# Kernel optimization log

Hardware: AMD Instinct MI355X
Metric: run time of the kernel (lower is better)

The kernel has to match this reference:

```python
import jax, jax.numpy as jnp
import numpy as np
import math

# hyperparams matching init_kwargs
GAMMA_S = 0.8
GAMMA_U = 0.8
RHO_I = 0.1
RHO_T = 0.1
EPS = 1e-10
TAU_MIN = 0.005
TAU_MAX = 1.0
TAU_INIT = 0.07
GRAD_CLIP = 5.0
ETA_INIT = 0.01
ETA_MIN = 0.0001
N_STATE = 2900000
BSZ = 4096
DIM = 1024


def setup_inputs() -> dict:
    key = jax.random.key(0)
    k1, k2 = jax.random.split(key)
    imf = jax.random.normal(k1, (BSZ, DIM), jnp.float32)
    imf = imf / jnp.linalg.norm(imf, axis=1, keepdims=True)
    txf = jax.random.normal(k2, (BSZ, DIM), jnp.float32)
    txf = txf / jnp.linalg.norm(txf, axis=1, keepdims=True)
    return {
        "image_features": imf,
        "text_features": txf,
        "s_I": jnp.zeros((N_STATE,), jnp.float32),
        "s_T": jnp.zeros((N_STATE,), jnp.float32),
        "tau_I": jnp.full((N_STATE,), TAU_INIT, jnp.float32),
        "tau_T": jnp.full((N_STATE,), TAU_INIT, jnp.float32),
        "u_I": jnp.zeros((N_STATE,), jnp.float32),
        "u_T": jnp.zeros((N_STATE,), jnp.float32),
        "b_I": jnp.zeros((N_STATE,), jnp.float32),
        "b_T": jnp.zeros((N_STATE,), jnp.float32),
        "image_ids": jnp.arange(BSZ, dtype=jnp.int32),
        "text_ids": jnp.arange(BSZ, dtype=jnp.int32),
        "epoch": 5,
        "max_epoch": 30,
    }


def reference(image_features, text_features, s_I, s_T, tau_I, tau_T,
              u_I, u_T, b_I, b_T, image_ids, text_ids, epoch, max_epoch):
    B = image_features.shape[0]
    sim = jnp.einsum('id,jd->ij', image_features, text_features)  # [B,B]
    diag_sim = jnp.diagonal(sim)                                  # [B]

    tau_image = tau_I[image_ids]  # [B]
    tau_text = tau_T[text_ids]    # [B]

    image_diffs = sim - diag_sim[:, None]
    text_diffs = sim - diag_sim[None, :]
    # .detach() in torch -> stop_gradient
    idt = jax.lax.stop_gradient(image_diffs / tau_image[:, None])
    tdt = jax.lax.stop_gradient(text_diffs / tau_text[None, :])

    # max-trick state b_I / b_T: running row/col max per sample id
    old_b_I = b_I[image_ids]
    new_b_I = jnp.maximum(jnp.max(idt, axis=1), old_b_I)  # [B]
    old_b_T = b_T[text_ids]
    new_b_T = jnp.maximum(jnp.max(tdt, axis=0), old_b_T)  # [B]

    exp_image_diffs = jnp.exp(idt - new_b_I[:, None])
    exp_text_diffs = jnp.exp(tdt - new_b_T[None, :])
    g_I = jnp.sum(exp_image_diffs, axis=1, keepdims=True) / (B - 1)  # [B,1]
    g_T = jnp.sum(exp_text_diffs, axis=0, keepdims=True) / (B - 1)   # [1,B]

    # moving-average s state (compute_last=False, last_g_* = None path)
    s_I_new = (1.0 - GAMMA_S) * s_I[image_ids] * jnp.exp(old_b_I - new_b_I) + GAMMA_S * g_I[:, 0]
    s_T_new = (1.0 - GAMMA_S) * s_T[text_ids] * jnp.exp(old_b_T - new_b_T) + GAMMA_S * g_T[0, :]
    s_I_b = s_I_new[:, None]  # same shape as g_I
    s_T_b = s_T_new[None, :]  # same shape as g_T

    weights_image = exp_image_diffs / (s_I_b + EPS)
    weights_text = exp_text_diffs / (s_T_b + EPS)

    image_loss = jnp.sum(weights_image * image_diffs, axis=1, keepdims=True) / (B - 1)
    text_loss = jnp.sum(weights_text * text_diffs, axis=0, keepdims=True) / (B - 1)
    total_loss = image_loss.mean() + text_loss.mean()

    grad_tau_image = (jnp.log(s_I_b) + new_b_I[:, None] + RHO_I
                      - jnp.sum(weights_image * idt, axis=1, keepdims=True) / (B - 1))
    grad_tau_text = (jnp.log(s_T_b) + new_b_T[None, :] + RHO_T
                     - jnp.sum(weights_text * tdt, axis=0, keepdims=True) / (B - 1))

    u_I_new = (1.0 - GAMMA_U) * u_I[image_ids] + GAMMA_U * jnp.clip(grad_tau_image[:, 0], -GRAD_CLIP, GRAD_CLIP)
    u_T_new = (1.0 - GAMMA_U) * u_T[text_ids] + GAMMA_U * jnp.clip(grad_tau_text[0, :], -GRAD_CLIP, GRAD_CLIP)

    eta_cur = ETA_MIN + (ETA_INIT - ETA_MIN) * math.cos(math.pi * (epoch / max_epoch) / 2)
    tau_I_new = jnp.clip(tau_image - eta_cur * u_I_new, TAU_MIN, TAU_MAX)
    tau_T_new = jnp.clip(tau_text - eta_cur * u_T_new, TAU_MIN, TAU_MAX)

    # scattered state writes (the module's in-place buffer updates)
    b_I_out = b_I.at[image_ids].set(new_b_I)
    b_T_out = b_T.at[text_ids].set(new_b_T)
    s_I_out = s_I.at[image_ids].set(s_I_new)
    s_T_out = s_T.at[text_ids].set(s_T_new)
    u_I_out = u_I.at[image_ids].set(u_I_new)
    u_T_out = u_T.at[text_ids].set(u_T_new)
    tau_I_out = tau_I.at[image_ids].set(tau_I_new)
    tau_T_out = tau_T.at[text_ids].set(tau_T_new)

    avg_image_tau = tau_image.mean()
    avg_text_tau = tau_text.mean()

    return (g_I, g_T, grad_tau_image, grad_tau_text, total_loss,
            avg_image_tau, avg_text_tau,
            s_I_out, s_T_out, u_I_out, u_T_out,
            b_I_out, b_T_out, tau_I_out, tau_T_out)
```

## Files before the change

kernel.cpp:

```cpp
#include <hip/hip_runtime.h>
#include <math.h>

#define BSZ 4096
#define DIM 1024
#define NST 2900000

constexpr float GAMMA_S   = 0.8f;
constexpr float GAMMA_U   = 0.8f;
constexpr float RHO_I_C   = 0.1f;
constexpr float RHO_T_C   = 0.1f;
constexpr float C_EPS     = 1e-10f;
constexpr float TAU_MIN_C = 0.005f;
constexpr float TAU_MAX_C = 1.0f;
constexpr float GCLIP     = 5.0f;
constexpr float ETA_INIT_C = 0.01f;
constexpr float ETA_MIN_C  = 1e-4f;
constexpr float PI_F       = 3.14159265358979323846f;

typedef __bf16 bf16x8 __attribute__((ext_vector_type(8)));
typedef float  f32x4  __attribute__((ext_vector_type(4)));

__device__ __forceinline__ unsigned short f2bf(float f) {
    unsigned int u = __float_as_uint(f);
    u += 0x7fffu + ((u >> 16) & 1u);
    return (unsigned short)(u >> 16);
}
__device__ __forceinline__ float bf2f(unsigned short s) {
    return __uint_as_float(((unsigned int)s) << 16);
}

__global__ __launch_bounds__(256) void conv_diag(const float* __restrict__ imf,
                                                 const float* __restrict__ txf,
                                                 unsigned short* __restrict__ abf,
                                                 unsigned short* __restrict__ bbf,
                                                 const float* __restrict__ tau_I,
                                                 const float* __restrict__ tau_T,
                                                 const float* __restrict__ b_I,
                                                 const float* __restrict__ b_T,
                                                 const int* __restrict__ iid,
                                                 const int* __restrict__ tid_,
                                                 float* diag, float* tauIg, float* tauTg,
                                                 float* obI, float* obT,
                                                 float* __restrict__ scal) {
    if (blockIdx.x == 0 && threadIdx.x < 3) scal[threadIdx.x] = 0.f;
    const int w  = threadIdx.x >> 6;
    const int ln = threadIdx.x & 63;
    const int i  = blockIdx.x * 4 + w;
    float dot = 0.f;
#pragma unroll
    for (int k = 0; k < 4; ++k) {
        const int off = i * DIM + k * 256 + ln * 4;
        float4 a = *(const float4*)&imf[off];
        float4 b = *(const float4*)&txf[off];
        ushort4 ra, rb;
        ra.x = f2bf(a.x); ra.y = f2bf(a.y); ra.z = f2bf(a.z); ra.w = f2bf(a.w);
        rb.x = f2bf(b.x); rb.y = f2bf(b.y); rb.z = f2bf(b.z); rb.w = f2bf(b.w);
        *(ushort4*)&abf[off] = ra;
        *(ushort4*)&bbf[off] = rb;
        dot += bf2f(ra.x) * bf2f(rb.x) + bf2f(ra.y) * bf2f(rb.y) +
               bf2f(ra.z) * bf2f(rb.z) + bf2f(ra.w) * bf2f(rb.w);
    }
#pragma unroll
    for (int m = 32; m; m >>= 1) dot += __shfl_xor(dot, m);
    if (ln == 0) {
        diag[i] = dot;
        const int id = iid[i];
        tauIg[i] = tau_I[id];
        obI[i]   = b_I[id];
        const int td = tid_[i];
        tauTg[i] = tau_T[td];
        obT[i]   = b_T[td];
    }
}

__device__ __forceinline__ void async16(const void* g, void* l) {
    __builtin_amdgcn_global_load_lds(
        (const __attribute__((address_space(1))) void*)g,
        (__attribute__((address_space(3))) void*)l, 16, 0, 0);
}

__global__ __launch_bounds__(256) void gemm_fused(const unsigned short* __restrict__ A,
                                                  const unsigned short* __restrict__ B,
                                                  const float* __restrict__ diag,
                                                  const float* __restrict__ tauIg,
                                                  const float* __restrict__ tauTg,
                                                  float* __restrict__ rpM,
                                                  float* __restrict__ rpE,
                                                  float* __restrict__ rpV,
                                                  float* __restrict__ cpM,
                                                  float* __restrict__ cpE,
                                                  float* __restrict__ cpV,
                                                  const float* __restrict__ s_I,
                                                  const float* __restrict__ s_T,
                                                  const float* __restrict__ u_I,
                                                  const float* __restrict__ u_T,
                                                  const float* __restrict__ b_I,
                                                  const float* __restrict__ b_T,
                                                  const float* __restrict__ tau_I,
                                                  const float* __restrict__ tau_T,
                                                  float* __restrict__ outbase) {
    __shared__ unsigned short As[128 * 32];
    __shared__ unsigned short Bs[128 * 32];

    const int tid = threadIdx.x;
    const int gid = ((blockIdx.x >> 4) << 3) | (blockIdx.x & 7);

    if ((blockIdx.x >> 3) & 1) {
        const size_t idx = (size_t)gid * 256 + tid;
        const size_t stride = (size_t)1024 * 256;
        const size_t NV = (NST - 1) / 4;
        const float* srcs[8] = {s_I, s_T, u_I, u_T, b_I, b_T, tau_I, tau_T};
#pragma unroll
        for (int a = 0; a < 8; ++a) {
            const float* s = srcs[a];
            float* d = outbase + (size_t)a * NST;
            for (size_t cidx = idx; cidx < NV; cidx += stride) {
                const size_t e = 1 + 4 * cidx;
                float4 v = make_float4(s[e], s[e + 1], s[e + 2], s[e + 3]);
                *(float4*)&d[e] = v;
            }
            if (idx == 0) d[0] = s[0];
            if (idx < 3)  d[NST - 3 + idx] = s[NST - 3 + idx];
        }
        return;
    }

    const int bjIdx = gid & 31, biIdx = gid >> 5;
    const int bi = biIdx * 128;
    const int bj = bjIdx * 128;
    const int lane = tid & 63;
    const int wave = tid >> 6;
    const int m_base = (wave >> 1) * 64;
    const int n_base = (wave & 1) * 64;

    const int c0 = tid, c1 = tid + 256;
    const int r0 = c0 >> 2, kg0 = ((c0 & 3) ^ ((r0 >> 1) & 3)) * 8;
    const int r1 = c1 >> 2, kg1 = ((c1 & 3) ^ ((r1 >> 1) & 3)) * 8;

    f32x4 acc[4][4];
#pragma unroll
    for (int m = 0; m < 4; ++m)
#pragma unroll
        for (int n = 0; n < 4; ++n)
            acc[m][n] = (f32x4){0.f, 0.f, 0.f, 0.f};

    const int mrow = lane & 15;
    const int q    = lane >> 4;

    for (int k0 = 0; k0 < DIM; k0 += 32) {
        __syncthreads();
        async16(&A[(size_t)(bi + r0) * DIM + k0 + kg0], &As[c0 * 8]);
        async16(&A[(size_t)(bi + r1) * DIM + k0 + kg1], &As[c1 * 8]);
        async16(&B[(size_t)(bj + r0) * DIM + k0 + kg0], &Bs[c0 * 8]);
        async16(&B[(size_t)(bj + r1) * DIM + k0 + kg1], &Bs[c1 * 8]);
        __syncthreads();

        bf16x8 af[4], bfr[4];
#pragma unroll
        for (int t = 0; t < 4; ++t) {
            const int rlA = m_base + t * 16 + mrow;
            const int rlB = n_base + t * 16 + mrow;
            af[t]  = *(const bf16x8*)&As[rlA * 32 + (q ^ ((rlA >> 1) & 3)) * 8];
            bfr[t] = *(const bf16x8*)&Bs[rlB * 32 + (q ^ ((rlB >> 1) & 3)) * 8];
        }
#pragma unroll
        for (int mt = 0; mt < 4; ++mt)
#pragma unroll
            for (int nt = 0; nt < 4; ++nt)
                acc[mt][nt] = __builtin_amdgcn_mfma_f32_16x16x32_bf16(
                    af[mt], bfr[nt], acc[mt][nt], 0, 0, 0);
    }

    __syncthreads();
    float* prm = (float*)Bs;
    if (tid < 128) {
        prm[tid]       = diag[bi + tid];
        prm[128 + tid] = 1.0f / tauIg[bi + tid];
        prm[256 + tid] = diag[bj + tid];
        prm[384 + tid] = 1.0f / tauTg[bj + tid];
    }
    __syncthreads();

    float* red = (float*)As;
    const int rowq = (lane >> 4) * 4;

#pragma unroll
    for (int mt = 0; mt < 4; ++mt)
#pragma unroll
        for (int r = 0; r < 4; ++r) {
            const int row_l = m_base + mt * 16 + rowq + r;
            const float dgr = prm[row_l];
            const float itr = prm[128 + row_l];
            float v0 = (acc[mt][0][r] - dgr) * itr;
            float v1 = (acc[mt][1][r] - dgr) * itr;
            float v2 = (acc[mt][2][r] - dgr) * itr;
            float v3 = (acc[mt][3][r] - dgr) * itr;
            float m = fmaxf(fmaxf(v0, v1), fmaxf(v2, v3));
#pragma unroll
            for (int x = 1; x <= 8; x <<= 1) m = fmaxf(m, __shfl_xor(m, x));
            const float e0 = __expf(v0 - m), e1 = __expf(v1 - m);
            const float e2 = __expf(v2 - m), e3 = __expf(v3 - m);
            float se = e0 + e1 + e2 + e3;
            float sv = e0 * v0 + e1 * v1 + e2 * v2 + e3 * v3;
#pragma unroll
            for (int x = 1; x <= 8; x <<= 1) {
                se += __shfl_xor(se, x);
                sv += __shfl_xor(sv, x);
            }
            if ((lane & 15) == 0) {
                const int idx = wave * 64 + mt * 16 + rowq + r;
                red[idx] = m; red[256 + idx] = se; red[512 + idx] = sv;
            }
        }

#pragma unroll
    for (int nt = 0; nt < 4; ++nt) {
        const int col_l = n_base + nt * 16 + (lane & 15);
        const float dgc = prm[256 + col_l];
        const float itc = prm[384 + col_l];
        float m = -INFINITY;
#pragma unroll
        for (int mt = 0; mt < 4; ++mt)
#pragma unroll
            for (int r = 0; r < 4; ++r)
                m = fmaxf(m, (acc[mt][nt][r] - dgc) * itc);
        m = fmaxf(m, __shfl_xor(m, 16));
        m = fmaxf(m, __shfl_xor(m, 32));
        float se = 0.f, sv = 0.f;
#pragma unroll
        for (int mt = 0; mt < 4; ++mt)
#pragma unroll
            for (int r = 0; r < 4; ++r) {
                const float v = (acc[mt][nt][r] - dgc) * itc;
                const float e = __expf(v - m);
                se += e; sv += e * v;
            }
        se += __shfl_xor(se, 16); se += __shfl_xor(se, 32);
        sv += __shfl_xor(sv, 16); sv += __shfl_xor(sv, 32);
        if (lane < 16) {
            const int idx = wave * 64 + nt * 16 + lane;
            red[768 + idx] = m; red[1024 + idx] = se; red[1280 + idx] = sv;
        }
    }
    __syncthreads();

    if (tid < 128) {
        const int rg = tid, li = rg & 63;
        const int w0 = (rg >> 6) * 2, w1 = w0 + 1;
        const float mA = red[w0 * 64 + li], mB = red[w1 * 64 + li];
        const float M = fmaxf(mA, mB);
        const float fA = __expf(mA - M), fB = __expf(mB - M);
        const size_t o = (size_t)bjIdx * BSZ + bi + rg;
        rpM[o] = M;
        rpE[o] = red[256 + w0 * 64 + li] * fA + red[256 + w1 * 64 + li] * fB;
        rpV[o] = red[512 + w0 * 64 + li] * fA + red[512 + w1 * 64 + li] * fB;
    } else {
        const int cg = tid - 128, li = cg & 63;
        const int w0 = cg >> 6, w1 = w0 + 2;
        const float mA = red[768 + w0 * 64 + li], mB = red[768 + w1 * 64 + li];
        const float M = fmaxf(mA, mB);
        const float fA = __expf(mA - M), fB = __expf(mB - M);
        const size_t o = (size_t)biIdx * BSZ + bj + cg;
        cpM[o] = M;
        cpE[o] = red[1024 + w0 * 64 + li] * fA + red[1024 + w1 * 64 + li] * fB;
        cpV[o] = red[1280 + w0 * 64 + li] * fA + red[1280 + w1 * 64 + li] * fB;
    }
}

__global__ __launch_bounds__(256) void finalize(const float* __restrict__ s_I,
                                                const float* __restrict__ s_T,
                                                const float* __restrict__ u_I,
                                                const float* __restrict__ u_T,
                                                const int* __restrict__ iid,
                                                const int* __restrict__ tid_,
                                                const int* __restrict__ epoch,
                                                const int* __restrict__ maxep,
                                                const float* __restrict__ tauIg,
                                                const float* __restrict__ tauTg,
                                                const float* __restrict__ obI,
                                                const float* __restrict__ obT,
                                                const float* __restrict__ rpM,
                                                const float* __restrict__ rpE,
                                                const float* __restrict__ rpV,
                                                const float* __restrict__ cpM,
                                                const float* __restrict__ cpE,
                                                const float* __restrict__ cpV,
                                                float* __restrict__ out) {
    const int i = blockIdx.x * 256 + threadIdx.x;

    const float eta = ETA_MIN_C + (ETA_INIT_C - ETA_MIN_C) *
                      cosf(0.5f * PI_F * ((float)epoch[0] / (float)maxep[0]));
    const float invBm1 = 1.0f / (float)(BSZ - 1);
    const float invB   = 1.0f / (float)BSZ;

    float* o_gI   = out;
    float* o_gT   = out + BSZ;
    float* o_gti  = out + 2 * BSZ;
    float* o_gtt  = out + 3 * BSZ;
    float* o_sI   = out + 4 * BSZ + 3;
    float* o_sT   = o_sI + NST;
    float* o_uI   = o_sT + NST;
    float* o_uT   = o_uI + NST;
    float* o_bI   = o_uT + NST;
    float* o_bT   = o_bI + NST;
    float* o_tauI = o_bT + NST;
    float* o_tauT = o_tauI + NST;

    float lossc, tI_B, tT_B;

    {
        const int id = iid[i];
        float mr = -INFINITY;
#pragma unroll
        for (int k = 0; k < 32; ++k) mr = fmaxf(mr, rpM[(size_t)k * BSZ + i]);
        const float tau = tauIg[i];
        const float ob = obI[i];
        const float nb = fmaxf(ob, mr);
        float se = 0.f, sv = 0.f;
#pragma unroll
        for (int k = 0; k < 32; ++k) {
            const float f = __expf(rpM[(size_t)k * BSZ + i] - nb);
            se += rpE[(size_t)k * BSZ + i] * f;
            sv += rpV[(size_t)k * BSZ + i] * f;
        }
        const float g = se * invBm1;
        const float s_new = (1.f - GAMMA_S) * s_I[id] * __expf(ob - nb) + GAMMA_S * g;
        const float W = sv * invBm1 / (s_new + C_EPS);
        const float grad = logf(s_new) + nb + RHO_I_C - W;
        lossc = tau * W;
        tI_B  = tau * invB;
        const float gc = fminf(fmaxf(grad, -GCLIP), GCLIP);
        const float u_new = (1.f - GAMMA_U) * u_I[id] + GAMMA_U * gc;
        const float tau_new = fminf(fmaxf(tau - eta * u_new, TAU_MIN_C), TAU_MAX_C);
        o_gI[i] = g;
        o_gti[i] = grad;
        o_sI[id] = s_new;
        o_uI[id] = u_new;
        o_bI[id] = nb;
        o_tauI[id] = tau_new;
    }
    {
        const int id = tid_[i];
        float mc = -INFINITY;
#pragma unroll
        for (int k = 0; k < 32; ++k) mc = fmaxf(mc, cpM[(size_t)k * BSZ + i]);
        const float tau = tauTg[i];
        const float ob = obT[i];
        const float nb = fmaxf(ob, mc);
        float se = 0.f, sv = 0.f;
#pragma unroll
        for (int k = 0; k < 32; ++k) {
            const float f = __expf(cpM[(size_t)k * BSZ + i] - nb);
            se += cpE[(size_t)k * BSZ + i] * f;
            sv += cpV[(size_t)k * BSZ + i] * f;
        }
        const float g = se * invBm1;
        const float s_new = (1.f - GAMMA_S) * s_T[id] * __expf(ob - nb) + GAMMA_S * g;
        const float W = sv * invBm1 / (s_new + C_EPS);
        const float grad = logf(s_new) + nb + RHO_T_C - W;
        lossc += tau * W;
        tT_B   = tau * invB;
        const float gc = fminf(fmaxf(grad, -GCLIP), GCLIP);
        const float u_new = (1.f - GAMMA_U) * u_T[id] + GAMMA_U * gc;
        const float tau_new = fminf(fmaxf(tau - eta * u_new, TAU_MIN_C), TAU_MAX_C);
        o_gT[i] = g;
        o_gtt[i] = grad;
        o_sT[id] = s_new;
        o_uT[id] = u_new;
        o_bT[id] = nb;
        o_tauT[id] = tau_new;
    }

    float v0 = lossc * invB, v1 = tI_B, v2 = tT_B;
#pragma unroll
    for (int o = 32; o; o >>= 1) {
        v0 += __shfl_down(v0, o);
        v1 += __shfl_down(v1, o);
        v2 += __shfl_down(v2, o);
    }
    __shared__ float lds[4][3];
    const int wv = threadIdx.x >> 6, ln = threadIdx.x & 63;
    if (ln == 0) { lds[wv][0] = v0; lds[wv][1] = v1; lds[wv][2] = v2; }
    __syncthreads();
    if (threadIdx.x == 0) {
        atomicAdd(&out[4 * BSZ + 0], lds[0][0] + lds[1][0] + lds[2][0] + lds[3][0]);
        atomicAdd(&out[4 * BSZ + 1], lds[0][1] + lds[1][1] + lds[2][1] + lds[3][1]);
        atomicAdd(&out[4 * BSZ + 2], lds[0][2] + lds[1][2] + lds[2][2] + lds[3][2]);
    }
}

extern "C" void kernel_launch(void* const* d_in, const int* in_sizes, int n_in,
                              void* d_out, int out_size, void* d_ws, size_t ws_size,
                              hipStream_t stream) {
    const float* imf   = (const float*)d_in[0];
    const float* txf   = (const float*)d_in[1];
    const float* s_I   = (const float*)d_in[2];
    const float* s_T   = (const float*)d_in[3];
    const float* tau_I = (const float*)d_in[4];
    const float* tau_T = (const float*)d_in[5];
    const float* u_I   = (const float*)d_in[6];
    const float* u_T   = (const float*)d_in[7];
    const float* b_I   = (const float*)d_in[8];
    const float* b_T   = (const float*)d_in[9];
    const int* iid     = (const int*)d_in[10];
    const int* tid_    = (const int*)d_in[11];
    const int* epoch   = (const int*)d_in[12];
    const int* maxep   = (const int*)d_in[13];

    float* out = (float*)d_out;
    float* ws  = (float*)d_ws;

    float* diag  = ws + 0 * BSZ;
    float* tauIg = ws + 1 * BSZ;
    float* tauTg = ws + 2 * BSZ;
    float* obI   = ws + 3 * BSZ;
    float* obT   = ws + 4 * BSZ;
    float* rpM   = ws + 5 * BSZ;
    float* rpE   = rpM + (size_t)32 * BSZ;
    float* rpV   = rpE + (size_t)32 * BSZ;
    float* cpM   = rpV + (size_t)32 * BSZ;
    float* cpE   = cpM + (size_t)32 * BSZ;
    float* cpV   = cpE + (size_t)32 * BSZ;
    unsigned short* abf = (unsigned short*)(cpV + (size_t)32 * BSZ);
    unsigned short* bbf = abf + (size_t)BSZ * DIM;

    conv_diag<<<BSZ / 4, 256, 0, stream>>>(imf, txf, abf, bbf, tau_I, tau_T, b_I, b_T,
                                           iid, tid_, diag, tauIg, tauTg, obI, obT,
                                           out + 4 * BSZ);
    gemm_fused<<<2048, 256, 0, stream>>>(abf, bbf, diag, tauIg, tauTg,
                                         rpM, rpE, rpV, cpM, cpE, cpV,
                                         s_I, s_T, u_I, u_T, b_I, b_T, tau_I, tau_T,
                                         out + 4 * BSZ + 3);
    finalize<<<BSZ / 256, 256, 0, stream>>>(s_I, s_T, u_I, u_T, iid, tid_, epoch, maxep,
                                            tauIg, tauTg, obI, obT,
                                            rpM, rpE, rpV, cpM, cpE, cpV, out);
}
```

Before: 286.0 us.

## Move state-buffer copy from GEMM kernel into conversion kernel

The bulk copy of the eight 2.9M-element state arrays used to run in half of the GEMM grid's blocks, interleaved with the tiles. It now runs inside the bf16 conversion/diagonal kernel, so the GEMM launches only its 1024 compute blocks with a plain block index. This changes the cross-kernel schedule: the memory-bound copy no longer overlaps the compute-bound GEMM and instead adds to the front kernel's traffic, which may lengthen the serial critical path.

```diff
diff --git a/kernel.cpp b/kernel.cpp
--- a/kernel.cpp
+++ b/kernel.cpp
@@ -29,7 +29,7 @@
     return __uint_as_float(((unsigned int)s) << 16);
 }
 
-__global__ __launch_bounds__(256) void conv_diag(const float* __restrict__ imf,
+__global__ __launch_bounds__(256) void conv_copy(const float* __restrict__ imf,
                                                  const float* __restrict__ txf,
                                                  unsigned short* __restrict__ abf,
                                                  unsigned short* __restrict__ bbf,
@@ -41,7 +41,12 @@
                                                  const int* __restrict__ tid_,
                                                  float* diag, float* tauIg, float* tauTg,
                                                  float* obI, float* obT,
-                                                 float* __restrict__ scal) {
+                                                 const float* __restrict__ s_I,
+                                                 const float* __restrict__ s_T,
+                                                 const float* __restrict__ u_I,
+                                                 const float* __restrict__ u_T,
+                                                 float* __restrict__ scal,
+                                                 float* __restrict__ outbase) {
     if (blockIdx.x == 0 && threadIdx.x < 3) scal[threadIdx.x] = 0.f;
     const int w  = threadIdx.x >> 6;
     const int ln = threadIdx.x & 63;
@@ -71,6 +76,23 @@
         tauTg[i] = tau_T[td];
         obT[i]   = b_T[td];
     }
+
+    const size_t idx = (size_t)blockIdx.x * 256 + threadIdx.x;
+    const size_t stride = (size_t)1024 * 256;
+    const size_t NV = (NST - 1) / 4;
+    const float* srcs[8] = {s_I, s_T, u_I, u_T, b_I, b_T, tau_I, tau_T};
+#pragma unroll
+    for (int a = 0; a < 8; ++a) {
+        const float* s = srcs[a];
+        float* d = outbase + (size_t)a * NST;
+        for (size_t cidx = idx; cidx < NV; cidx += stride) {
+            const size_t e = 1 + 4 * cidx;
+            float4 v = make_float4(s[e], s[e + 1], s[e + 2], s[e + 3]);
+            *(float4*)&d[e] = v;
+        }
+        if (idx == 0) d[0] = s[0];
+        if (idx < 3)  d[NST - 3 + idx] = s[NST - 3 + idx];
+    }
 }
 
 __device__ __forceinline__ void async16(const void* g, void* l) {
@@ -79,52 +101,22 @@
         (__attribute__((address_space(3))) void*)l, 16, 0, 0);
 }
 
-__global__ __launch_bounds__(256) void gemm_fused(const unsigned short* __restrict__ A,
-                                                  const unsigned short* __restrict__ B,
-                                                  const float* __restrict__ diag,
-                                                  const float* __restrict__ tauIg,
-                                                  const float* __restrict__ tauTg,
-                                                  float* __restrict__ rpM,
-                                                  float* __restrict__ rpE,
-                                                  float* __restrict__ rpV,
-                                                  float* __restrict__ cpM,
-                                                  float* __restrict__ cpE,
-                                                  float* __restrict__ cpV,
-                                                  const float* __restrict__ s_I,
-                                                  const float* __restrict__ s_T,
-                                                  const float* __restrict__ u_I,
-                                                  const float* __restrict__ u_T,
-                                                  const float* __restrict__ b_I,
-                                                  const float* __restrict__ b_T,
-                                                  const float* __restrict__ tau_I,
-                                                  const float* __restrict__ tau_T,
-                                                  float* __restrict__ outbase) {
+__global__ __launch_bounds__(256) void gemm_softmax(const unsigned short* __restrict__ A,
+                                                    const unsigned short* __restrict__ B,
+                                                    const float* __restrict__ diag,
+                                                    const float* __restrict__ tauIg,
+                                                    const float* __restrict__ tauTg,
+                                                    float* __restrict__ rpM,
+                                                    float* __restrict__ rpE,
+                                                    float* __restrict__ rpV,
+                                                    float* __restrict__ cpM,
+                                                    float* __restrict__ cpE,
+                                                    float* __restrict__ cpV) {
     __shared__ unsigned short As[128 * 32];
     __shared__ unsigned short Bs[128 * 32];
 
     const int tid = threadIdx.x;
-    const int gid = ((blockIdx.x >> 4) << 3) | (blockIdx.x & 7);
-
-    if ((blockIdx.x >> 3) & 1) {
-        const size_t idx = (size_t)gid * 256 + tid;
-        const size_t stride = (size_t)1024 * 256;
-        const size_t NV = (NST - 1) / 4;
-        const float* srcs[8] = {s_I, s_T, u_I, u_T, b_I, b_T, tau_I, tau_T};
-#pragma unroll
-        for (int a = 0; a < 8; ++a) {
-            const float* s = srcs[a];
-            float* d = outbase + (size_t)a * NST;
-            for (size_t cidx = idx; cidx < NV; cidx += stride) {
-                const size_t e = 1 + 4 * cidx;
-                float4 v = make_float4(s[e], s[e + 1], s[e + 2], s[e + 3]);
-                *(float4*)&d[e] = v;
-            }
-            if (idx == 0) d[0] = s[0];
-            if (idx < 3)  d[NST - 3 + idx] = s[NST - 3 + idx];
-        }
-        return;
-    }
-
+    const int gid = blockIdx.x;
     const int bjIdx = gid & 31, biIdx = gid >> 5;
     const int bi = biIdx * 128;
     const int bj = bjIdx * 128;
@@ -424,13 +416,12 @@
     unsigned short* abf = (unsigned short*)(cpV + (size_t)32 * BSZ);
     unsigned short* bbf = abf + (size_t)BSZ * DIM;
 
-    conv_diag<<<BSZ / 4, 256, 0, stream>>>(imf, txf, abf, bbf, tau_I, tau_T, b_I, b_T,
+    conv_copy<<<BSZ / 4, 256, 0, stream>>>(imf, txf, abf, bbf, tau_I, tau_T, b_I, b_T,
                                            iid, tid_, diag, tauIg, tauTg, obI, obT,
-                                           out + 4 * BSZ);
-    gemm_fused<<<2048, 256, 0, stream>>>(abf, bbf, diag, tauIg, tauTg,
-                                         rpM, rpE, rpV, cpM, cpE, cpV,
-                                         s_I, s_T, u_I, u_T, b_I, b_T, tau_I, tau_T,
-                                         out + 4 * BSZ + 3);
+                                           s_I, s_T, u_I, u_T,
+                                           out + 4 * BSZ, out + 4 * BSZ + 3);
+    gemm_softmax<<<1024, 256, 0, stream>>>(abf, bbf, diag, tauIg, tauTg,
+                                           rpM, rpE, rpV, cpM, cpE, cpV);
     finalize<<<BSZ / 256, 256, 0, stream>>>(s_I, s_T, u_I, u_T, iid, tid_, epoch, maxep,
                                             tauIg, tauTg, obI, obT,
                                             rpM, rpE, rpV, cpM, cpE, cpV, out);
```

Result: no change. 291.6 us (+2.0%).
